# Performance work log

Measured on AMD Instinct MI355X. Metric: run time of the kernel, lower is better.

The kernel has to match this reference:

```python
import jax, jax.numpy as jnp
import numpy as np

GRID_SIZE = 64
K = 3
GRID_RANGE = (-1.0, 1.0)
NUM_BASIS = GRID_SIZE + K


def _knots():
    # extended knot vector: k repeats of the left end, uniform grid, k repeats of the right end
    g = jnp.linspace(GRID_RANGE[0], GRID_RANGE[1], GRID_SIZE + 1, dtype=jnp.float32)
    left = jnp.full((K,), GRID_RANGE[0], dtype=jnp.float32)
    right = jnp.full((K,), GRID_RANGE[1], dtype=jnp.float32)
    return jnp.concatenate([left, g, right])  # (GRID_SIZE + 2K + 1,)


def reference(x):
    """Cox-de Boor B-spline basis, bottom-up DP (vectorized over batch).

    x: (B,) float32 -> (B, NUM_BASIS) float32
    """
    knots = _knots()
    n0 = GRID_SIZE + 2 * K  # number of degree-0 basis functions
    xb = x[:, None]  # (B, 1)
    # degree 0: indicator of half-open interval [t_i, t_{i+1})
    N = ((xb >= knots[None, :n0]) & (xb < knots[None, 1:n0 + 1])).astype(x.dtype)
    for d in range(1, K + 1):
        n = n0 - d  # number of degree-d bases
        t_i = knots[:n]
        t_id = knots[d:d + n]
        t_i1 = knots[1:1 + n]
        t_id1 = knots[d + 1:d + 1 + n]
        den1 = t_id - t_i
        den2 = t_id1 - t_i1
        # term is dropped entirely when the denominator is zero (repeated knots)
        w1 = jnp.where(den1 != 0, (xb - t_i) / jnp.where(den1 != 0, den1, 1.0), 0.0)
        w2 = jnp.where(den2 != 0, (t_id1 - xb) / jnp.where(den2 != 0, den2, 1.0), 0.0)
        N = w1 * N[:, :n] + w2 * N[:, 1:n + 1]
    return N  # (B, NUM_BASIS)


def setup_inputs() -> dict:
    key = jax.random.key(0)
    x = jax.random.uniform(key, (2_000_000,), minval=-1.0, maxval=1.0, dtype=jnp.float32)
    return {"x": x}
```

## Files before the change

### kernel.cpp

```cpp
#include <hip/hip_runtime.h>

#define NUM_BASIS 67
#define ROWS_PER_BLOCK 512
#define BLOCK_THREADS 256
#define TILE_VEC4 (ROWS_PER_BLOCK * NUM_BASIS / 4)

typedef float f32x4 __attribute__((ext_vector_type(4)));

__device__ __forceinline__ float kv(int i) {
    i = min(max(i, 3), 67);
    return (float)(i - 35) * 0.03125f;
}

__device__ __forceinline__ void row_basis(float xv, int& m, float N[4]) {
    N[0] = N[1] = N[2] = N[3] = 0.0f;
    m = 1 << 20;
    if (xv >= -1.0f && xv < 1.0f) {
        int cell = (int)floorf((xv + 1.0f) * 32.0f);
        cell = min(max(cell, 0), 63);
        m = cell + 3;
        while (m > 3 && xv < kv(m)) --m;
        while (m < 66 && xv >= kv(m + 1)) ++m;

        float left[4], right[4];
        N[0] = 1.0f;
#pragma unroll
        for (int d = 1; d <= 3; ++d) {
            left[d] = xv - kv(m + 1 - d);
            right[d] = kv(m + d) - xv;
            float saved = 0.0f;
#pragma unroll
            for (int r = 0; r < d; ++r) {
                float temp = __fdividef(N[r], right[r + 1] + left[d - r]);
                N[r] = saved + right[r + 1] * temp;
                saved = left[d - r] * temp;
            }
            N[d] = saved;
        }
    }
}

__device__ __forceinline__ float pick(int d, f32x4 n) {
    float v = 0.0f;
    v = (d == 0) ? n.x : v;
    v = (d == 1) ? n.y : v;
    v = (d == 2) ? n.z : v;
    v = (d == 3) ? n.w : v;
    return v;
}

__global__ __launch_bounds__(BLOCK_THREADS) void SplineBasis_kernel(
        const float* __restrict__ x, float* __restrict__ out, int B) {
    __shared__ int s_m[ROWS_PER_BLOCK];
    __shared__ f32x4 s_N[ROWS_PER_BLOCK];
    const int tid = threadIdx.x;
    const int blockRow0 = blockIdx.x * ROWS_PER_BLOCK;

    for (int r = tid; r < ROWS_PER_BLOCK; r += BLOCK_THREADS) {
        int m = 1 << 20;
        float N[4] = {0.f, 0.f, 0.f, 0.f};
        const int row = blockRow0 + r;
        if (row < B) row_basis(x[row], m, N);
        s_m[r] = m;
        s_N[r] = (f32x4){N[0], N[1], N[2], N[3]};
    }
    __syncthreads();

    const int rows = min(ROWS_PER_BLOCK, B - blockRow0);
    if (rows == ROWS_PER_BLOCK) {
        f32x4* o4 = (f32x4*)(out + (size_t)blockRow0 * NUM_BASIS);
        for (int i = tid; i < TILE_VEC4; i += BLOCK_THREADS) {
            const int g = i * 4;
            const int r0 = (int)((unsigned)g / NUM_BASIS);
            const int c0 = g - r0 * NUM_BASIS;
            const int r1 = min(r0 + 1, ROWS_PER_BLOCK - 1);
            const int m0 = s_m[r0];
            const int m1 = s_m[r1];
            const f32x4 n0 = s_N[r0];
            const f32x4 n1 = s_N[r1];
            f32x4 v;
            int c;
            c = c0 + 0; v.x = (c < NUM_BASIS) ? pick(c - m0 + 3, n0) : pick(c - NUM_BASIS - m1 + 3, n1);
            c = c0 + 1; v.y = (c < NUM_BASIS) ? pick(c - m0 + 3, n0) : pick(c - NUM_BASIS - m1 + 3, n1);
            c = c0 + 2; v.z = (c < NUM_BASIS) ? pick(c - m0 + 3, n0) : pick(c - NUM_BASIS - m1 + 3, n1);
            c = c0 + 3; v.w = (c < NUM_BASIS) ? pick(c - m0 + 3, n0) : pick(c - NUM_BASIS - m1 + 3, n1);
            __builtin_nontemporal_store(v, o4 + i);
        }
    } else if (rows > 0) {
        const int n = rows * NUM_BASIS;
        float* o = out + (size_t)blockRow0 * NUM_BASIS;
        for (int i = tid; i < n; i += BLOCK_THREADS) {
            const int r0 = (int)((unsigned)i / NUM_BASIS);
            const int c0 = i - r0 * NUM_BASIS;
            o[i] = pick(c0 - s_m[r0] + 3, s_N[r0]);
        }
    }
}

extern "C" void kernel_launch(void* const* d_in, const int* in_sizes, int n_in,
                              void* d_out, int out_size, void* d_ws, size_t ws_size,
                              hipStream_t stream) {
    const float* x = (const float*)d_in[0];
    float* out = (float*)d_out;
    const int B = in_sizes[0];
    const int nblocks = (B + ROWS_PER_BLOCK - 1) / ROWS_PER_BLOCK;
    SplineBasis_kernel<<<nblocks, BLOCK_THREADS, 0, stream>>>(x, out, B);
}
```

Measured before the change: 543.1 us.

## Split spline basis into row-compute and grid-stride expand kernels via workspace

Replaces the single fused kernel with two launches when workspace is large enough. The first computes each row's four nonzero basis values and span index into global workspace. The second is a persistent grid-stride kernel over the flattened output that writes vectorized nontemporal stores, so the store stream is decoupled from per-block compute and barriers. This adds a second launch plus a workspace round trip of roughly 40 MB, and a serial single-thread tail loop. The fallback fused path uses 128-row tiles with scalar stores.

```diff
diff --git a/kernel.cpp b/kernel.cpp
--- a/kernel.cpp
+++ b/kernel.cpp
@@ -1,9 +1,7 @@
 #include <hip/hip_runtime.h>
 
 #define NUM_BASIS 67
-#define ROWS_PER_BLOCK 512
 #define BLOCK_THREADS 256
-#define TILE_VEC4 (ROWS_PER_BLOCK * NUM_BASIS / 4)
 
 typedef float f32x4 __attribute__((ext_vector_type(4)));
 
@@ -49,51 +47,73 @@
     return v;
 }
 
-__global__ __launch_bounds__(BLOCK_THREADS) void SplineBasis_kernel(
+__global__ __launch_bounds__(BLOCK_THREADS) void SplineRow_kernel(
+        const float* __restrict__ x, f32x4* __restrict__ wsN,
+        int* __restrict__ wsM, int B) {
+    const int r = blockIdx.x * BLOCK_THREADS + threadIdx.x;
+    if (r < B) {
+        int m;
+        float N[4];
+        row_basis(x[r], m, N);
+        wsN[r] = (f32x4){N[0], N[1], N[2], N[3]};
+        wsM[r] = m;
+    }
+}
+
+__global__ __launch_bounds__(BLOCK_THREADS) void SplineExpand_kernel(
+        const f32x4* __restrict__ wsN, const int* __restrict__ wsM,
+        f32x4* __restrict__ out4, int n4, int out_size, int B) {
+    const int stride = gridDim.x * BLOCK_THREADS;
+    const int t0 = blockIdx.x * BLOCK_THREADS + threadIdx.x;
+    for (int i = t0; i < n4; i += stride) {
+        const int g = i * 4;
+        const int r0 = (int)((unsigned)g / NUM_BASIS);
+        const int c0 = g - r0 * NUM_BASIS;
+        const int r1 = min(r0 + 1, B - 1);
+        const int m0 = wsM[r0];
+        const int m1 = wsM[r1];
+        const f32x4 n0 = wsN[r0];
+        const f32x4 n1 = wsN[r1];
+        f32x4 v;
+        int c;
+        c = c0 + 0; v.x = (c < NUM_BASIS) ? pick(c - m0 + 3, n0) : pick(c - NUM_BASIS - m1 + 3, n1);
+        c = c0 + 1; v.y = (c < NUM_BASIS) ? pick(c - m0 + 3, n0) : pick(c - NUM_BASIS - m1 + 3, n1);
+        c = c0 + 2; v.z = (c < NUM_BASIS) ? pick(c - m0 + 3, n0) : pick(c - NUM_BASIS - m1 + 3, n1);
+        c = c0 + 3; v.w = (c < NUM_BASIS) ? pick(c - m0 + 3, n0) : pick(c - NUM_BASIS - m1 + 3, n1);
+        __builtin_nontemporal_store(v, out4 + i);
+    }
+    if (t0 == 0) {
+        float* out = (float*)out4;
+        for (int g = n4 * 4; g < out_size; ++g) {
+            const int r0 = (int)((unsigned)g / NUM_BASIS);
+            const int c0 = g - r0 * NUM_BASIS;
+            out[g] = pick(c0 - wsM[r0] + 3, wsN[r0]);
+        }
+    }
+}
+
+__global__ __launch_bounds__(BLOCK_THREADS) void SplineFused_kernel(
         const float* __restrict__ x, float* __restrict__ out, int B) {
-    __shared__ int s_m[ROWS_PER_BLOCK];
-    __shared__ f32x4 s_N[ROWS_PER_BLOCK];
+    __shared__ int s_m[128];
+    __shared__ f32x4 s_N[128];
     const int tid = threadIdx.x;
-    const int blockRow0 = blockIdx.x * ROWS_PER_BLOCK;
-
-    for (int r = tid; r < ROWS_PER_BLOCK; r += BLOCK_THREADS) {
+    const int blockRow0 = blockIdx.x * 128;
+    if (tid < 128) {
         int m = 1 << 20;
         float N[4] = {0.f, 0.f, 0.f, 0.f};
-        const int row = blockRow0 + r;
+        const int row = blockRow0 + tid;
         if (row < B) row_basis(x[row], m, N);
-        s_m[r] = m;
-        s_N[r] = (f32x4){N[0], N[1], N[2], N[3]};
+        s_m[tid] = m;
+        s_N[tid] = (f32x4){N[0], N[1], N[2], N[3]};
     }
     __syncthreads();
-
-    const int rows = min(ROWS_PER_BLOCK, B - blockRow0);
-    if (rows == ROWS_PER_BLOCK) {
-        f32x4* o4 = (f32x4*)(out + (size_t)blockRow0 * NUM_BASIS);
-        for (int i = tid; i < TILE_VEC4; i += BLOCK_THREADS) {
-            const int g = i * 4;
-            const int r0 = (int)((unsigned)g / NUM_BASIS);
-            const int c0 = g - r0 * NUM_BASIS;
-            const int r1 = min(r0 + 1, ROWS_PER_BLOCK - 1);
-            const int m0 = s_m[r0];
-            const int m1 = s_m[r1];
-            const f32x4 n0 = s_N[r0];
-            const f32x4 n1 = s_N[r1];
-            f32x4 v;
-            int c;
-            c = c0 + 0; v.x = (c < NUM_BASIS) ? pick(c - m0 + 3, n0) : pick(c - NUM_BASIS - m1 + 3, n1);
-            c = c0 + 1; v.y = (c < NUM_BASIS) ? pick(c - m0 + 3, n0) : pick(c - NUM_BASIS - m1 + 3, n1);
-            c = c0 + 2; v.z = (c < NUM_BASIS) ? pick(c - m0 + 3, n0) : pick(c - NUM_BASIS - m1 + 3, n1);
-            c = c0 + 3; v.w = (c < NUM_BASIS) ? pick(c - m0 + 3, n0) : pick(c - NUM_BASIS - m1 + 3, n1);
-            __builtin_nontemporal_store(v, o4 + i);
-        }
-    } else if (rows > 0) {
-        const int n = rows * NUM_BASIS;
-        float* o = out + (size_t)blockRow0 * NUM_BASIS;
-        for (int i = tid; i < n; i += BLOCK_THREADS) {
-            const int r0 = (int)((unsigned)i / NUM_BASIS);
-            const int c0 = i - r0 * NUM_BASIS;
-            o[i] = pick(c0 - s_m[r0] + 3, s_N[r0]);
-        }
+    const int rows = min(128, B - blockRow0);
+    const int n = rows * NUM_BASIS;
+    float* o = out + (size_t)blockRow0 * NUM_BASIS;
+    for (int i = tid; i < n; i += BLOCK_THREADS) {
+        const int r0 = (int)((unsigned)i / NUM_BASIS);
+        const int c0 = i - r0 * NUM_BASIS;
+        o[i] = pick(c0 - s_m[r0] + 3, s_N[r0]);
     }
 }
 
@@ -101,8 +121,18 @@
                               void* d_out, int out_size, void* d_ws, size_t ws_size,
                               hipStream_t stream) {
     const float* x = (const float*)d_in[0];
-    float* out = (float*)d_out;
     const int B = in_sizes[0];
-    const int nblocks = (B + ROWS_PER_BLOCK - 1) / ROWS_PER_BLOCK;
-    SplineBasis_kernel<<<nblocks, BLOCK_THREADS, 0, stream>>>(x, out, B);
+    const size_t needed = (size_t)B * 16 + (size_t)B * 4;
+    if (ws_size >= needed) {
+        f32x4* wsN = (f32x4*)d_ws;
+        int* wsM = (int*)((char*)d_ws + (size_t)B * 16);
+        const int g1 = (B + BLOCK_THREADS - 1) / BLOCK_THREADS;
+        SplineRow_kernel<<<g1, BLOCK_THREADS, 0, stream>>>(x, wsN, wsM, B);
+        const int n4 = out_size / 4;
+        SplineExpand_kernel<<<2048, BLOCK_THREADS, 0, stream>>>(
+            wsN, wsM, (f32x4*)d_out, n4, out_size, B);
+    } else {
+        const int nblocks = (B + 127) / 128;
+        SplineFused_kernel<<<nblocks, BLOCK_THREADS, 0, stream>>>(x, (float*)d_out, B);
+    }
 }
```

New measurement: 544.6 us. Within noise of the previous version (+0.3%).
